# Kernel tuning notes

Hardware: AMD Instinct MI355X
Metric: run time of the kernel (lower is better)

Reference implementation:

```python
import jax, jax.numpy as jnp
import numpy as np
from jax import lax

STRIDES = (4, 8, 16, 32, 64)
SIZES = (32, 64, 128, 256, 512)
RATIOS = (0.5, 1.0, 2.0)
IMG_H, IMG_W = 1024, 1024
PRE_NMS = 1000
POST_NMS = 1000
NMS_THRESH = 0.7
BBOX_CLIP = float(np.log(1000.0 / 16.0))
NEG_INF = -1e9


def _cell_anchors(size):
    a = []
    for r in RATIOS:
        w = size * np.sqrt(1.0 / r)
        h = size * np.sqrt(r)
        a.append([-w / 2.0, -h / 2.0, w / 2.0, h / 2.0])
    return np.array(a, np.float32)  # [A,4]


def _level_anchors(H, W, stride, size):
    cell = _cell_anchors(size)  # [A,4]
    ys = np.arange(H, dtype=np.float32) * stride
    xs = np.arange(W, dtype=np.float32) * stride
    yy, xx = np.meshgrid(ys, xs, indexing='ij')  # row-major (H,W)
    shifts = np.stack([xx, yy, xx, yy], axis=-1).reshape(-1, 1, 4)
    return jnp.asarray((shifts + cell[None]).reshape(-1, 4))  # [(H*W*A),4] in (H,W,A) order


def conv2d(x, w, b, pad):
    y = lax.conv_general_dilated(x, w, (1, 1), pad,
                                 dimension_numbers=('NCHW', 'OIHW', 'NCHW'))
    return y + b[None, :, None, None]


def decode(deltas, anchors):
    widths = anchors[:, 2] - anchors[:, 0] + 1.0
    heights = anchors[:, 3] - anchors[:, 1] + 1.0
    ctr_x = anchors[:, 0] + 0.5 * widths
    ctr_y = anchors[:, 1] + 0.5 * heights
    dx, dy = deltas[..., 0], deltas[..., 1]
    dw = jnp.minimum(deltas[..., 2], BBOX_CLIP)
    dh = jnp.minimum(deltas[..., 3], BBOX_CLIP)
    pcx = dx * widths + ctr_x
    pcy = dy * heights + ctr_y
    pw = jnp.exp(dw) * widths
    ph = jnp.exp(dh) * heights
    return jnp.stack([pcx - 0.5 * pw, pcy - 0.5 * ph,
                      pcx + 0.5 * pw - 1.0, pcy + 0.5 * ph - 1.0], axis=-1)


def iou_matrix(boxes):
    area = (boxes[:, 2] - boxes[:, 0]) * (boxes[:, 3] - boxes[:, 1])
    lt = jnp.maximum(boxes[:, None, :2], boxes[None, :, :2])
    rb = jnp.minimum(boxes[:, None, 2:], boxes[None, :, 2:])
    wh = jnp.maximum(rb - lt, 0.0)
    inter = wh[..., 0] * wh[..., 1]
    return inter / (area[:, None] + area[None, :] - inter + 1e-9)


def nms_keep(boxes):
    # boxes [N,4] already sorted by score desc; greedy NMS -> bool keep mask
    N = boxes.shape[0]
    iou = iou_matrix(boxes)

    def body(keep, i):
        row = jnp.take(iou, i, axis=0) > NMS_THRESH
        row = row.at[i].set(False)
        keep = jnp.where(keep[i], keep & ~row, keep)
        return keep, None

    keep, _ = lax.scan(body, jnp.ones((N,), bool), jnp.arange(N))
    return keep


def _forward(feats, conv_w, conv_b, cls_w, cls_b, bbox_w, bbox_b):
    level_boxes, level_scores = [], []
    for lvl, feat in enumerate(feats):
        B, _, H, W = feat.shape
        t = jax.nn.relu(conv2d(feat, conv_w, conv_b, 'SAME'))
        logits = conv2d(t, cls_w, cls_b, 'VALID')    # [B,A,H,W]
        breg = conv2d(t, bbox_w, bbox_b, 'VALID')    # [B,4A,H,W]
        A = logits.shape[1]
        scores = jnp.transpose(logits, (0, 2, 3, 1)).reshape(B, -1)            # (H,W,A)
        deltas = breg.reshape(B, A, 4, H, W).transpose(0, 3, 4, 1, 2).reshape(B, -1, 4)
        anchors = _level_anchors(H, W, STRIDES[lvl], SIZES[lvl])
        boxes = decode(deltas, anchors)  # [B,N,4]
        boxes = jnp.stack([jnp.clip(boxes[..., 0], 0.0, IMG_W - 1.0),
                           jnp.clip(boxes[..., 1], 0.0, IMG_H - 1.0),
                           jnp.clip(boxes[..., 2], 0.0, IMG_W - 1.0),
                           jnp.clip(boxes[..., 3], 0.0, IMG_H - 1.0)], axis=-1)
        k = min(PRE_NMS, scores.shape[1])
        top_s, idx = lax.top_k(scores, k)                                   # [B,k]
        top_b = jnp.take_along_axis(boxes, idx[..., None], axis=1)          # [B,k,4]
        keep = jax.vmap(nms_keep)(top_b)                                    # [B,k] bool
        level_scores.append(jnp.where(keep, top_s, NEG_INF))
        level_boxes.append(top_b)
    all_s = jnp.concatenate(level_scores, axis=1)
    all_b = jnp.concatenate(level_boxes, axis=1)
    fs, fi = lax.top_k(all_s, POST_NMS)                                     # [B,POST]
    fb = jnp.take_along_axis(all_b, fi[..., None], axis=1)                  # [B,POST,4]
    return jnp.concatenate([fb, fs[..., None]], axis=-1)                    # [B,POST,5]


def setup_inputs() -> dict:
    key = jax.random.key(0)
    ks = jax.random.split(key, 8)
    C = 256
    feats = {
        'feat0': jax.random.normal(ks[0], (2, C, 256, 256), jnp.float32),
        'feat1': jax.random.normal(ks[1], (2, C, 128, 128), jnp.float32),
        'feat2': jax.random.normal(ks[2], (2, C, 64, 64), jnp.float32),
        'feat3': jax.random.normal(ks[3], (2, C, 32, 32), jnp.float32),
        'feat4': jax.random.normal(ks[4], (2, C, 16, 16), jnp.float32),
    }
    params = {
        'conv_w': jax.random.normal(ks[5], (C, C, 3, 3), jnp.float32) * 0.01,
        'conv_b': jnp.zeros((C,), jnp.float32),
        'cls_w': jax.random.normal(ks[6], (3, C, 1, 1), jnp.float32) * 0.01,
        'cls_b': jnp.zeros((3,), jnp.float32),
        'bbox_w': jax.random.normal(ks[7], (12, C, 1, 1), jnp.float32) * 0.01,
        'bbox_b': jnp.zeros((12,), jnp.float32),
    }
    return {**feats, **params}


def reference(feat0, feat1, feat2, feat3, feat4, conv_w, conv_b, cls_w, cls_b, bbox_w, bbox_b):
    return _forward([feat0, feat1, feat2, feat3, feat4],
                    conv_w, conv_b, cls_w, cls_b, bbox_w, bbox_b)
```

## Files before the change

### kernel.cpp

```cpp
#include <hip/hip_runtime.h>
#include <cmath>


#define NTOT_PER_IMG 261888
#define ATOT_PER_IMG 4768

__constant__ int c_NLVL[5] = {196608, 49152, 12288, 3072, 768};
__constant__ int c_KLVL[5] = {1000, 1000, 1000, 1000, 768};
__constant__ int c_LOFF[5] = {0, 196608, 245760, 258048, 261120};
__constant__ int c_AOFF[5] = {0, 1000, 2000, 3000, 4000};

struct Anch { float cx1[3]; float cy1[3]; };
struct ConvCfg { Anch an[5]; };

__device__ __forceinline__ void ldsBarrier() {
  asm volatile("s_waitcnt lgkmcnt(0)" ::: "memory");
  __builtin_amdgcn_s_barrier();
  asm volatile("" ::: "memory");
}

__global__ __launch_bounds__(256) void wtrans(const float* __restrict__ Wsrc,
                                              float* __restrict__ Wt) {
  __shared__ float T[16][17];
  int k0 = blockIdx.x * 16;
  int o0 = blockIdx.y * 16;
  int i = threadIdx.x >> 4, j = threadIdx.x & 15;
  T[i][j] = Wsrc[(size_t)(o0 + i) * 2304 + (k0 + j)];
  __syncthreads();
  Wt[(size_t)(k0 + i) * 256 + (o0 + j)] = T[j][i];
}

__global__ __launch_bounds__(256, 2) void conv_gemm(
    const float* __restrict__ f0, const float* __restrict__ f1,
    const float* __restrict__ f2, const float* __restrict__ f3,
    const float* __restrict__ f4, const float* __restrict__ Wt,
    const float* __restrict__ convb, const float* __restrict__ clsw,
    const float* __restrict__ clsb, const float* __restrict__ bboxw,
    const float* __restrict__ bboxb, float* __restrict__ scoresOut,
    float4* __restrict__ boxesOut, ConvCfg cfg) {
  __shared__ __align__(16) float s_mem[4096];
  __shared__ float s_Red2[272];
  float* const s_x = s_mem;
  float* const s_tl = s_mem;

  int b = blockIdx.x;
  const float* feat;
  int lvl, img, tile, H, logW, stride, lvlOff;
  if (b < 2048) {
    lvl = 0; feat = f0; H = 256; logW = 8; stride = 4; lvlOff = 0;
    img = b >> 10; tile = b & 1023;
  } else if (b < 2560) {
    lvl = 1; feat = f1; H = 128; logW = 7; stride = 8; lvlOff = 196608;
    int r = b - 2048; img = r >> 8; tile = r & 255;
  } else if (b < 2688) {
    lvl = 2; feat = f2; H = 64; logW = 6; stride = 16; lvlOff = 245760;
    int r = b - 2560; img = r >> 6; tile = r & 63;
  } else if (b < 2720) {
    lvl = 3; feat = f3; H = 32; logW = 5; stride = 32; lvlOff = 258048;
    int r = b - 2688; img = r >> 4; tile = r & 15;
  } else {
    lvl = 4; feat = f4; H = 16; logW = 4; stride = 64; lvlOff = 261120;
    int r = b - 2720; img = r >> 2; tile = r & 3;
  }
  const int W = H, HW = H * W;
  const int p0 = tile * 64;
  const float* fimg = feat + (size_t)img * 256 * HW;

  const int log2nc = (logW < 6) ? logW : 6;
  const int ncols = 1 << log2nc;
  const int R = 64 >> log2nc;
  const int py0 = p0 >> logW;
  const int c_start = p0 & (W - 1);
  const int WIN = ncols + 2;
  const int NX = (R + 2) * WIN;

  const int tid = threadIdx.x;
  const int oc0 = (tid >> 3) * 8;
  const int pxg = tid & 7;
  const int px0 = pxg * 8;
  const int trow = px0 >> log2nc;
  const int tcol0 = px0 & (ncols - 1);

  int goffX = -1, loffX = -1;
  if (tid < NX) {
    int lr = tid / WIN;
    int lc = tid - lr * WIN;
    int sy = py0 - 1 + lr;
    int sx = c_start - 1 + lc;
    loffX = lr * 68 + lc;
    if (sy >= 0 && sy < H && sx >= 0 && sx < W) goffX = sy * W + sx;
  }

  float acc[8][8];
#pragma unroll
  for (int i = 0; i < 8; i++)
#pragma unroll
    for (int p = 0; p < 8; p++) acc[i][p] = 0.f;

  if (loffX >= 0) s_x[loffX] = (goffX >= 0) ? fimg[goffX] : 0.f;
  ldsBarrier();

#pragma unroll 1
  for (int ic = 0; ic < 256; ic++) {
    const float* xb = s_x + (ic & 1) * 408;

    float pxv;
    if (ic < 255) {
      const float* fnext = fimg + (size_t)(ic + 1) * HW;
      pxv = (goffX >= 0) ? fnext[goffX] : 0.f;
    }

    const float* wic = Wt + (size_t)ic * 2304 + oc0;
#pragma unroll 1
    for (int ky = 0; ky < 3; ky++) {
      const float* xr = xb + (trow + ky) * 68 + tcol0;
      float4 xA = *(const float4*)(xr);
      float4 xB = *(const float4*)(xr + 4);
      float2 xC = *(const float2*)(xr + 8);
      float xw[10] = {xA.x, xA.y, xA.z, xA.w,
                      xB.x, xB.y, xB.z, xB.w, xC.x, xC.y};
      const float* wky = wic + ky * 768;
#pragma unroll
      for (int kx = 0; kx < 3; kx++) {
        float4 wa = *(const float4*)(wky + kx * 256);
        float4 wc = *(const float4*)(wky + kx * 256 + 4);
        float wv[8] = {wa.x, wa.y, wa.z, wa.w, wc.x, wc.y, wc.z, wc.w};
#pragma unroll
        for (int i = 0; i < 8; i++)
#pragma unroll
          for (int p = 0; p < 8; p++)
            acc[i][p] = __builtin_fmaf(wv[i], xw[p + kx], acc[i][p]);
      }
    }

    if (ic < 255) {
      float* xn = s_x + ((ic + 1) & 1) * 408;
      if (loffX >= 0) xn[loffX] = pxv;
    }
    ldsBarrier();
  }

  float cb[8];
#pragma unroll
  for (int i = 0; i < 8; i++) cb[i] = convb[oc0 + i];

  const Anch an = cfg.an[lvl];
  const float BCLIP = (float)4.135166556742356;
  const size_t obase = (size_t)img * NTOT_PER_IMG + lvlOff;

#pragma unroll 1
  for (int r = 0; r < 4; r++) {
    if ((pxg >> 1) == r) {
      int pl = px0 - 16 * r;
#pragma unroll
      for (int p = 0; p < 8; p++) {
        float4 v0 = make_float4(fmaxf(acc[0][p] + cb[0], 0.f),
                                fmaxf(acc[1][p] + cb[1], 0.f),
                                fmaxf(acc[2][p] + cb[2], 0.f),
                                fmaxf(acc[3][p] + cb[3], 0.f));
        float4 v1 = make_float4(fmaxf(acc[4][p] + cb[4], 0.f),
                                fmaxf(acc[5][p] + cb[5], 0.f),
                                fmaxf(acc[6][p] + cb[6], 0.f),
                                fmaxf(acc[7][p] + cb[7], 0.f));
        *(float4*)(s_tl + (pl + p) * 256 + oc0) = v0;
        *(float4*)(s_tl + (pl + p) * 256 + oc0 + 4) = v1;
      }
    }
    __syncthreads();

    if (tid < 240) {
      int px = tid / 15, c = tid - px * 15;
      const float* wr0 = (c < 3) ? (clsw + c * 256) : (bboxw + (c - 3) * 256);
      float bb = (c < 3) ? clsb[c] : bboxb[c - 3];
      const float* trow2 = &s_tl[px * 256];
      float tot = 0.f;
#pragma unroll
      for (int g = 0; g < 16; g++) {
        const float* wr = wr0 + g * 16;
        const float* tr = trow2 + g * 16;
        float s = 0.f;
#pragma unroll
        for (int i = 0; i < 16; i++) s += wr[i] * tr[i];
        tot += s;
      }
      s_Red2[px * 17 + c] = tot + bb;
    }
    __syncthreads();

    if (tid < 48) {
      int px = tid / 3, a = tid - px * 3;
      int pxl = p0 + r * 16 + px;
      int gy = pxl >> logW, gx = pxl & (W - 1);
      float sc = s_Red2[px * 17 + a];
      float dxv = s_Red2[px * 17 + 3 + a * 4 + 0];
      float dyv = s_Red2[px * 17 + 3 + a * 4 + 1];
      float dwv = s_Red2[px * 17 + 3 + a * 4 + 2];
      float dhv = s_Red2[px * 17 + 3 + a * 4 + 3];
      float sx = (float)(gx * stride), sy = (float)(gy * stride);
      float x1 = __fadd_rn(sx, an.cx1[a]);
      float x2 = __fsub_rn(sx, an.cx1[a]);
      float y1 = __fadd_rn(sy, an.cy1[a]);
      float y2 = __fsub_rn(sy, an.cy1[a]);
      float wdt = __fadd_rn(__fsub_rn(x2, x1), 1.0f);
      float hgt = __fadd_rn(__fsub_rn(y2, y1), 1.0f);
      float ctx = __fadd_rn(x1, __fmul_rn(0.5f, wdt));
      float cty = __fadd_rn(y1, __fmul_rn(0.5f, hgt));
      float dw = fminf(dwv, BCLIP), dh = fminf(dhv, BCLIP);
      float pcx = __fadd_rn(__fmul_rn(dxv, wdt), ctx);
      float pcy = __fadd_rn(__fmul_rn(dyv, hgt), cty);
      float pw = __fmul_rn(expf(dw), wdt);
      float ph = __fmul_rn(expf(dh), hgt);
      float hw = __fmul_rn(0.5f, pw), hh = __fmul_rn(0.5f, ph);
      float bx1 = __fsub_rn(pcx, hw);
      float by1 = __fsub_rn(pcy, hh);
      float bx2 = __fsub_rn(__fadd_rn(pcx, hw), 1.0f);
      float by2 = __fsub_rn(__fadd_rn(pcy, hh), 1.0f);
      bx1 = fminf(fmaxf(bx1, 0.f), 1023.f);
      by1 = fminf(fmaxf(by1, 0.f), 1023.f);
      bx2 = fminf(fmaxf(bx2, 0.f), 1023.f);
      by2 = fminf(fmaxf(by2, 0.f), 1023.f);
      size_t o = obase + (size_t)pxl * 3 + a;
      scoresOut[o] = sc;
      boxesOut[o] = make_float4(bx1, by1, bx2, by2);
    }
    __syncthreads();
  }
}

__device__ __forceinline__ unsigned fkey(float f) {
  unsigned b = __float_as_uint(f);
  return (b & 0x80000000u) ? ~b : (b | 0x80000000u);
}
__device__ __forceinline__ float funkey(unsigned u) {
  unsigned b = (u & 0x80000000u) ? (u & 0x7fffffffu) : ~u;
  return __uint_as_float(b);
}

template <bool FINAL>
__global__ __launch_bounds__(1024) void topk_kernel(
    const float* __restrict__ scoresIn, const float4* __restrict__ boxesIn,
    float* __restrict__ scoresOut, float4* __restrict__ boxesOut,
    float* __restrict__ finalOut) {
  __shared__ unsigned long long keys[1024];
  __shared__ unsigned hist[256];
  __shared__ unsigned s_comm[4];
  int lvl = 0, img, N, k;
  const float* src;
  const float4* bsrc;
  if (FINAL) {
    img = blockIdx.x; N = ATOT_PER_IMG; k = 1000;
    src = scoresIn + (size_t)img * ATOT_PER_IMG;
    bsrc = boxesIn + (size_t)img * ATOT_PER_IMG;
  } else {
    lvl = blockIdx.x; img = blockIdx.y;
    N = c_NLVL[lvl]; k = c_KLVL[lvl];
    src = scoresIn + (size_t)img * NTOT_PER_IMG + c_LOFF[lvl];
    bsrc = boxesIn + (size_t)img * NTOT_PER_IMG + c_LOFF[lvl];
  }
  const int tid = threadIdx.x;

  unsigned pref = 0, pmask = 0, krem = (unsigned)k, cntT = 0;
  for (int pass = 3; pass >= 0; pass--) {
    int shift = pass * 8;
    if (tid < 256) hist[tid] = 0;
    __syncthreads();
    for (int i = tid; i < N; i += 1024) {
      unsigned u = fkey(src[i]);
      if ((u & pmask) == pref) atomicAdd(&hist[(u >> shift) & 255], 1u);
    }
    __syncthreads();
    if (tid == 0) {
      unsigned cum = 0;
      for (int d = 255; d >= 0; d--) {
        unsigned c = hist[d];
        if (cum + c >= krem) {
          s_comm[0] = krem - cum; s_comm[1] = c; s_comm[2] = (unsigned)d;
          break;
        }
        cum += c;
      }
    }
    __syncthreads();
    krem = s_comm[0]; cntT = s_comm[1];
    pref |= s_comm[2] << shift;
    pmask |= 0xFFu << shift;
    __syncthreads();
  }
  const unsigned T = pref, r = krem;
  unsigned m = (unsigned)N;
  if (r < cntT) {
    unsigned lo = 0, hi = (unsigned)N;
    while (lo < hi) {
      unsigned mid = (lo + hi) >> 1;
      if (tid == 0) s_comm[3] = 0;
      __syncthreads();
      for (unsigned i = tid; i < mid; i += 1024)
        if (fkey(src[i]) == T) atomicAdd(&s_comm[3], 1u);
      __syncthreads();
      unsigned c = s_comm[3];
      __syncthreads();
      if (c >= r) hi = mid; else lo = mid + 1;
    }
    m = lo;
  }
  if (tid == 0) s_comm[3] = 0;
  __syncthreads();
  for (int i = tid; i < N; i += 1024) {
    unsigned u = fkey(src[i]);
    if (u > T || (u == T && (unsigned)i < m)) {
      unsigned p = atomicAdd(&s_comm[3], 1u);
      if (p < 1024)
        keys[p] = ((unsigned long long)u << 32) | (unsigned)(~(unsigned)i);
    }
  }
  __syncthreads();
  if (tid >= k) keys[tid] = 0ull;
  __syncthreads();
  for (unsigned k2 = 2; k2 <= 1024; k2 <<= 1) {
    for (unsigned j = k2 >> 1; j > 0; j >>= 1) {
      unsigned i = tid, ixj = i ^ j;
      if (ixj > i) {
        unsigned long long a = keys[i], b = keys[ixj];
        bool sw = ((i & k2) == 0) ? (a < b) : (a > b);
        if (sw) { keys[i] = b; keys[ixj] = a; }
      }
      __syncthreads();
    }
  }
  if (tid < k) {
    unsigned long long key = keys[tid];
    unsigned u = (unsigned)(key >> 32);
    unsigned idx = ~((unsigned)key);
    float sc = funkey(u);
    float4 b = bsrc[idx];
    if (FINAL) {
      float* o = finalOut + ((size_t)img * 1000 + tid) * 5;
      o[0] = b.x; o[1] = b.y; o[2] = b.z; o[3] = b.w; o[4] = sc;
    } else {
      scoresOut[(size_t)img * ATOT_PER_IMG + c_AOFF[lvl] + tid] = sc;
      boxesOut[(size_t)img * ATOT_PER_IMG + c_AOFF[lvl] + tid] = b;
    }
  }
}

__global__ __launch_bounds__(256) void nms_matrix(
    const float4* __restrict__ allb, unsigned long long* __restrict__ supp) {
  int lvl = blockIdx.x, img = blockIdx.y, rb = blockIdx.z;
  int k = c_KLVL[lvl];
  int task = img * 5 + lvl;
  const float4* src = allb + (size_t)img * ATOT_PER_IMG + c_AOFF[lvl];
  __shared__ float4 bb[1000];
  __shared__ float ar[1000];
  for (int j = threadIdx.x; j < k; j += 256) {
    float4 b = src[j];
    bb[j] = b;
    ar[j] = __fmul_rn(__fsub_rn(b.z, b.x), __fsub_rn(b.w, b.y));
  }
  __syncthreads();
  int i = rb * 256 + threadIdx.x;
  if (i < k) {
    float4 bi = bb[i];
    float ai = ar[i];
    unsigned long long* row = supp + ((size_t)task * 1024 + i) * 16;
    int jw0 = i >> 6;
    for (int jw = 0; jw < jw0; jw++) row[jw] = 0ull;
    for (int jw = jw0; jw < 16; jw++) {
      unsigned long long bits = 0;
      int jbase = jw * 64;
      for (int jj = 0; jj < 64; jj++) {
        int j = jbase + jj;
        if (j > i && j < k) {
          float4 bj = bb[j];
          float ltx = fmaxf(bi.x, bj.x), lty = fmaxf(bi.y, bj.y);
          float rbx = fminf(bi.z, bj.z), rby = fminf(bi.w, bj.w);
          float wx = fmaxf(__fsub_rn(rbx, ltx), 0.f);
          float wy = fmaxf(__fsub_rn(rby, lty), 0.f);
          float inter = __fmul_rn(wx, wy);
          float den = __fadd_rn(__fsub_rn(__fadd_rn(ai, ar[j]), inter), 1e-9f);
          if (__fdiv_rn(inter, den) > 0.7f) bits |= 1ull << jj;
        }
      }
      row[jw] = bits;
    }
  }
}

__global__ __launch_bounds__(64) void nms_scan(
    const float* __restrict__ topS, const unsigned long long* __restrict__ supp,
    float* __restrict__ fscore) {
  int lvl = blockIdx.x, img = blockIdx.y;
  int k = c_KLVL[lvl];
  int task = img * 5 + lvl;
  int lane = threadIdx.x;
  const unsigned long long* base = supp + (size_t)task * 1024 * 16;
  unsigned long long rem = 0, keep = 0;
  for (int b0 = 0; b0 < k; b0 += 16) {
    unsigned long long buf[16];
#pragma unroll
    for (int t = 0; t < 16; t++) {
      int i = b0 + t;
      buf[t] = (lane < 16 && i < k) ? base[(size_t)i * 16 + lane] : 0ull;
    }
#pragma unroll
    for (int t = 0; t < 16; t++) {
      int i = b0 + t;
      if (i >= k) break;
      int wi = i >> 6, bi = i & 63;
      unsigned long long rw = __shfl(rem, wi);
      if (!((rw >> bi) & 1ull)) {
        rem |= buf[t];
        if (lane == wi) keep |= (1ull << bi);
      }
    }
  }
  const float* ts = topS + (size_t)img * ATOT_PER_IMG + c_AOFF[lvl];
  float* fs = fscore + (size_t)img * ATOT_PER_IMG + c_AOFF[lvl];
  for (int i = lane; i < k; i += 64) {
    int wi = i >> 6;
    unsigned long long kw = __shfl(keep, wi);
    fs[i] = ((kw >> (i & 63)) & 1ull) ? ts[i] : -1e9f;
  }
}

static Anch mkAnch(double size) {
  Anch a;
  const double R[3] = {0.5, 1.0, 2.0};
  for (int i = 0; i < 3; i++) {
    double w = size * sqrt(1.0 / R[i]);
    double h = size * sqrt(R[i]);
    a.cx1[i] = (float)(-w / 2.0);
    a.cy1[i] = (float)(-h / 2.0);
  }
  return a;
}

extern "C" void kernel_launch(void* const* d_in, const int* in_sizes, int n_in,
                              void* d_out, int out_size, void* d_ws,
                              size_t ws_size, hipStream_t stream) {
  (void)in_sizes; (void)n_in; (void)out_size; (void)ws_size;
  const float* f0 = (const float*)d_in[0];
  const float* f1 = (const float*)d_in[1];
  const float* f2 = (const float*)d_in[2];
  const float* f3 = (const float*)d_in[3];
  const float* f4 = (const float*)d_in[4];
  const float* conv_w = (const float*)d_in[5];
  const float* conv_b = (const float*)d_in[6];
  const float* cls_w  = (const float*)d_in[7];
  const float* cls_b  = (const float*)d_in[8];
  const float* bbox_w = (const float*)d_in[9];
  const float* bbox_b = (const float*)d_in[10];
  float* out = (float*)d_out;

  float* wsf = (float*)d_ws;
  float* Wt     = wsf;
  float* scores = Wt + 589824;
  float* boxes  = scores + 2 * NTOT_PER_IMG;
  float* topS   = boxes + (size_t)2 * NTOT_PER_IMG * 4;
  float* allb   = topS + 2 * ATOT_PER_IMG;
  float* fscore = allb + (size_t)2 * ATOT_PER_IMG * 4;
  unsigned long long* supp =
      (unsigned long long*)(fscore + 2 * ATOT_PER_IMG);

  wtrans<<<dim3(144, 16), 256, 0, stream>>>(conv_w, Wt);

  ConvCfg cfg;
  const double SZ[5] = {32, 64, 128, 256, 512};
  for (int l = 0; l < 5; l++) cfg.an[l] = mkAnch(SZ[l]);

  conv_gemm<<<2728, 256, 0, stream>>>(f0, f1, f2, f3, f4, Wt, conv_b, cls_w,
                                      cls_b, bbox_w, bbox_b, scores,
                                      (float4*)boxes, cfg);

  topk_kernel<false><<<dim3(5, 2), 1024, 0, stream>>>(
      scores, (const float4*)boxes, topS, (float4*)allb, nullptr);
  nms_matrix<<<dim3(5, 2, 4), 256, 0, stream>>>((const float4*)allb, supp);
  nms_scan<<<dim3(5, 2), 64, 0, stream>>>(topS, supp, fscore);
  topk_kernel<true><<<2, 1024, 0, stream>>>(
      fscore, (const float4*)allb, nullptr, nullptr, out);
}
```

Baseline: 3.623 ms.

## Give each wavefront a private input tile copy to drop block barriers in conv loop

Each of the four wavefronts now loads and double-buffers its own copy of the input halo tile in LDS, so the per-input-channel block-wide s_barrier is replaced by a wave-local lgkmcnt wait. The intent is to remove 256 workgroup barriers per block and let waves drift independently. In exchange, each wave issues four times as many global feature loads and LDS stores per channel, LDS use grows (which may cut occupancy), and the epilogue tile row stride is padded to 260 to reduce bank conflicts.

After: 3.584 ms. Within noise of the previous version (-1.1%).

```diff
diff --git a/kernel.cpp b/kernel.cpp
--- a/kernel.cpp
+++ b/kernel.cpp
@@ -13,10 +13,8 @@
 struct Anch { float cx1[3]; float cy1[3]; };
 struct ConvCfg { Anch an[5]; };
 
-__device__ __forceinline__ void ldsBarrier() {
+__device__ __forceinline__ void ldsWaveFence() {
   asm volatile("s_waitcnt lgkmcnt(0)" ::: "memory");
-  __builtin_amdgcn_s_barrier();
-  asm volatile("" ::: "memory");
 }
 
 __global__ __launch_bounds__(256) void wtrans(const float* __restrict__ Wsrc,
@@ -38,10 +36,10 @@
     const float* __restrict__ clsb, const float* __restrict__ bboxw,
     const float* __restrict__ bboxb, float* __restrict__ scoresOut,
     float4* __restrict__ boxesOut, ConvCfg cfg) {
-  __shared__ __align__(16) float s_mem[4096];
+  __shared__ __align__(16) float s_mem[7424];
   __shared__ float s_Red2[272];
-  float* const s_x = s_mem;
   float* const s_tl = s_mem;
+  float* const s_xbase = s_mem + 4160;
 
   int b = blockIdx.x;
   const float* feat;
@@ -75,20 +73,29 @@
   const int NX = (R + 2) * WIN;
 
   const int tid = threadIdx.x;
+  const int wid = tid >> 6;
+  const int lane = tid & 63;
   const int oc0 = (tid >> 3) * 8;
   const int pxg = tid & 7;
   const int px0 = pxg * 8;
   const int trow = px0 >> log2nc;
   const int tcol0 = px0 & (ncols - 1);
 
-  int goffX = -1, loffX = -1;
-  if (tid < NX) {
-    int lr = tid / WIN;
-    int lc = tid - lr * WIN;
-    int sy = py0 - 1 + lr;
-    int sx = c_start - 1 + lc;
-    loffX = lr * 68 + lc;
-    if (sy >= 0 && sy < H && sx >= 0 && sx < W) goffX = sy * W + sx;
+  float* const s_xw = s_xbase + wid * 816;
+
+  int goffX[4], loffX[4];
+#pragma unroll
+  for (int s = 0; s < 4; s++) {
+    int idx = lane + 64 * s;
+    goffX[s] = -1; loffX[s] = -1;
+    if (idx < NX) {
+      int lr = idx / WIN;
+      int lc = idx - lr * WIN;
+      int sy = py0 - 1 + lr;
+      int sx = c_start - 1 + lc;
+      loffX[s] = lr * 68 + lc;
+      if (sy >= 0 && sy < H && sx >= 0 && sx < W) goffX[s] = sy * W + sx;
+    }
   }
 
   float acc[8][8];
@@ -97,17 +104,22 @@
 #pragma unroll
     for (int p = 0; p < 8; p++) acc[i][p] = 0.f;
 
-  if (loffX >= 0) s_x[loffX] = (goffX >= 0) ? fimg[goffX] : 0.f;
-  ldsBarrier();
+#pragma unroll
+  for (int s = 0; s < 4; s++)
+    if (loffX[s] >= 0)
+      s_xw[loffX[s]] = (goffX[s] >= 0) ? fimg[goffX[s]] : 0.f;
+  ldsWaveFence();
 
 #pragma unroll 1
   for (int ic = 0; ic < 256; ic++) {
-    const float* xb = s_x + (ic & 1) * 408;
-
-    float pxv;
+    const float* xb = s_xw + (ic & 1) * 408;
+
+    float pxv[4];
     if (ic < 255) {
       const float* fnext = fimg + (size_t)(ic + 1) * HW;
-      pxv = (goffX >= 0) ? fnext[goffX] : 0.f;
+#pragma unroll
+      for (int s = 0; s < 4; s++)
+        pxv[s] = (goffX[s] >= 0) ? fnext[goffX[s]] : 0.f;
     }
 
     const float* wic = Wt + (size_t)ic * 2304 + oc0;
@@ -134,10 +146,12 @@
     }
 
     if (ic < 255) {
-      float* xn = s_x + ((ic + 1) & 1) * 408;
-      if (loffX >= 0) xn[loffX] = pxv;
-    }
-    ldsBarrier();
+      float* xn = s_xw + ((ic + 1) & 1) * 408;
+#pragma unroll
+      for (int s = 0; s < 4; s++)
+        if (loffX[s] >= 0) xn[loffX[s]] = pxv[s];
+    }
+    ldsWaveFence();
   }
 
   float cb[8];
@@ -162,8 +176,8 @@
                                 fmaxf(acc[5][p] + cb[5], 0.f),
                                 fmaxf(acc[6][p] + cb[6], 0.f),
                                 fmaxf(acc[7][p] + cb[7], 0.f));
-        *(float4*)(s_tl + (pl + p) * 256 + oc0) = v0;
-        *(float4*)(s_tl + (pl + p) * 256 + oc0 + 4) = v1;
+        *(float4*)(s_tl + (pl + p) * 260 + oc0) = v0;
+        *(float4*)(s_tl + (pl + p) * 260 + oc0 + 4) = v1;
       }
     }
     __syncthreads();
@@ -172,7 +186,7 @@
       int px = tid / 15, c = tid - px * 15;
       const float* wr0 = (c < 3) ? (clsw + c * 256) : (bboxw + (c - 3) * 256);
       float bb = (c < 3) ? clsb[c] : bboxb[c - 3];
-      const float* trow2 = &s_tl[px * 256];
+      const float* trow2 = &s_tl[px * 260];
       float tot = 0.f;
 #pragma unroll
       for (int g = 0; g < 16; g++) {
```
